# Kernel optimization log

Measured on AMD Instinct MI355X. Metric: run time of the kernel, lower is better.

## Reference

```python
import jax, jax.numpy as jnp
import numpy as np

N_NODES = 100_000
N_FACES = 200_000
IN_CH = 128
OUT_CH = 29  # MLP out = OUT_CH + 3


def setup_inputs() -> dict:
    key = jax.random.key(0)
    k_pos, k_faces, k_ff, k_w1, k_w2 = jax.random.split(key, 5)
    pos = jax.random.normal(k_pos, (N_NODES, 3), dtype=jnp.float32)
    faces = jax.random.randint(k_faces, (N_FACES, 3), 0, N_NODES, dtype=jnp.int32)
    face_features = jax.random.normal(k_ff, (N_FACES, IN_CH), dtype=jnp.float32)
    d_in = IN_CH + 6
    W1 = jax.random.normal(k_w1, (d_in, IN_CH), dtype=jnp.float32) / np.sqrt(d_in)
    b1 = jnp.zeros((IN_CH,), dtype=jnp.float32)
    W2 = jax.random.normal(k_w2, (IN_CH, OUT_CH + 3), dtype=jnp.float32) / np.sqrt(IN_CH)
    b2 = jnp.zeros((OUT_CH + 3,), dtype=jnp.float32)
    return {"pos": pos, "face_features": face_features, "W1": W1, "b1": b1,
            "W2": W2, "b2": b2, "faces": faces}


def reference(pos, face_features, W1, b1, W2, b2, faces):
    def mlp(x):
        return jax.nn.relu(x @ W1 + b1) @ W2 + b2

    p0 = pos[faces[:, 0]]  # [F,3]
    p1 = pos[faces[:, 1]]
    p2 = pos[faces[:, 2]]

    g0 = mlp(jnp.concatenate([p1 - p0, p2 - p0, face_features], axis=1))
    g1 = mlp(jnp.concatenate([p2 - p1, p0 - p1, face_features], axis=1))
    g2 = mlp(jnp.concatenate([p0 - p2, p1 - p2, face_features], axis=1))

    face_features_out = (g0[:, 3:] + g1[:, 3:] + g2[:, 3:]) / 3.0  # [F,OUT_CH]

    # scatter_mean of per-corner deltas onto nodes; torch cat order matches
    # faces.T.flatten() = [faces[:,0], faces[:,1], faces[:,2]]
    vals = jnp.concatenate([g0[:, :3], g1[:, :3], g2[:, :3]], axis=0)  # [3F,3]
    idx = jnp.concatenate([faces[:, 0], faces[:, 1], faces[:, 2]], axis=0)  # [3F]
    sums = jax.ops.segment_sum(vals, idx, num_segments=N_NODES)
    counts = jax.ops.segment_sum(jnp.ones((vals.shape[0],), vals.dtype), idx,
                                 num_segments=N_NODES)
    delta_pos = sums / jnp.clip(counts, 1.0)[:, None]  # [N,3]

    new_pos = pos + delta_pos
    return (delta_pos, new_pos, face_features_out)
```

## Files before the change

### kernel.cpp

```cpp
#include <hip/hip_runtime.h>
#include <hip/hip_bf16.h>

#define N_NODES 100000
#define N_FACES 200000
#define FM 32
#define ROWS 96
#define NTILES (N_FACES / FM)
#define GRID 512
#define FS 136
#define ES 40
#define HS 136
#define W1K 160
#define W2K 128

typedef __attribute__((ext_vector_type(8))) short s8v;
typedef __attribute__((ext_vector_type(4))) short s4v;
typedef __attribute__((ext_vector_type(4))) float f4v;

static __device__ __forceinline__ short f2bf(float x) {
  __hip_bfloat16 h = __float2bfloat16(x);
  short s;
  __builtin_memcpy(&s, &h, 2);
  return s;
}

__global__ __launch_bounds__(256) void prep_kernel(
    const float* __restrict__ W1, const float* __restrict__ W2,
    short* __restrict__ w1t, short* __restrict__ w2t)
{
  int t = blockIdx.x * 256 + threadIdx.x;
  if (t < 128 * W1K) {
    int n = t / W1K, k = t % W1K;
    float v = 0.f;
    if (k < 128) v = W1[(k + 6) * 128 + n];
    else if (k < 134) v = W1[(k - 128) * 128 + n];
    w1t[t] = f2bf(v);
  }
  if (t < 32 * W2K) {
    int o = t / W2K, k = t % W2K;
    w2t[t] = f2bf(W2[k * 32 + o]);
  }
}

__global__ __launch_bounds__(512, 4) void face_kernel(
    const float* __restrict__ pos, const float* __restrict__ ffeat,
    const float* __restrict__ b1, const float* __restrict__ b2,
    const int* __restrict__ faces,
    const short* __restrict__ w1t_g, const short* __restrict__ w2t_g,
    float* __restrict__ out_ff, float* __restrict__ sums, int* __restrict__ cnt)
{
  __shared__ short xff[2][FM * FS];
  __shared__ short xe[2][ROWS * ES];
  __shared__ short hbuf[ROWS * HS];
  __shared__ int   nidb[2][ROWS];
  __shared__ float gsumb[FM * 30];

  const int t = threadIdx.x;
  const int lane = t & 63;
  const int wv = t >> 6;
  const int l15 = lane & 15;
  const int lq = lane >> 4;
  const int kq = lq * 8;
  const int nsel = wv & 1;

  s8v bw1[5], bw2[4];
#pragma unroll
  for (int kc = 0; kc < 5; ++kc)
    bw1[kc] = *(const s8v*)(w1t_g + (wv * 16 + l15) * W1K + kc * 32 + kq);
#pragma unroll
  for (int kk = 0; kk < 4; ++kk)
    bw2[kk] = *(const s8v*)(w2t_g + (nsel * 16 + l15) * W2K + kk * 32 + kq);
  const float b1j = b1[wv * 16 + l15];
  const float b2o = b2[nsel * 16 + l15];

  if (t < 2 * ROWS) {
    int b = t / ROWS, row = t - b * ROWS;
    s8v z = (s8v){0, 0, 0, 0, 0, 0, 0, 0};
    *(unsigned*)&xe[b][row * ES + 6] = 0u;
    *(s8v*)&xe[b][row * ES + 8] = z;
    *(s8v*)&xe[b][row * ES + 16] = z;
    *(s8v*)&xe[b][row * ES + 24] = z;
    *(s8v*)&xe[b][row * ES + 32] = z;
  }

  {
    int fb = blockIdx.x * FM;
    const float* fp = ffeat + ((size_t)(fb + (t >> 4)) << 7) + ((t & 15) << 3);
    f4v v0 = *(const f4v*)fp, v1 = *(const f4v*)(fp + 4);
    s8v s;
    s[0] = f2bf(v0.x); s[1] = f2bf(v0.y); s[2] = f2bf(v0.z); s[3] = f2bf(v0.w);
    s[4] = f2bf(v1.x); s[5] = f2bf(v1.y); s[6] = f2bf(v1.z); s[7] = f2bf(v1.w);
    *(s8v*)&xff[0][(t >> 4) * FS + ((t & 15) << 3)] = s;
    int rt = t - 384;
    if ((unsigned)rt < 96u) {
      int face = fb + (rt & 31), v = rt >> 5;
      int i0 = faces[face * 3 + 0], i1 = faces[face * 3 + 1], i2 = faces[face * 3 + 2];
      int ia = (v == 0) ? i0 : ((v == 1) ? i1 : i2);
      int ib = (v == 0) ? i1 : ((v == 1) ? i2 : i0);
      int ic = (v == 0) ? i2 : ((v == 1) ? i0 : i1);
      float ax = pos[ia * 3], ay = pos[ia * 3 + 1], az = pos[ia * 3 + 2];
      float bx = pos[ib * 3], by = pos[ib * 3 + 1], bz = pos[ib * 3 + 2];
      float cx = pos[ic * 3], cy = pos[ic * 3 + 1], cz = pos[ic * 3 + 2];
      s4v e;
      e[0] = f2bf(bx - ax); e[1] = f2bf(by - ay); e[2] = f2bf(bz - az); e[3] = f2bf(cx - ax);
      *(s4v*)&xe[0][rt * ES] = e;
      unsigned p2 = (unsigned)(unsigned short)f2bf(cy - ay) |
                    ((unsigned)(unsigned short)f2bf(cz - az) << 16);
      *(unsigned*)&xe[0][rt * ES + 4] = p2;
      nidb[0][rt] = ia;
    }
  }
  __syncthreads();

  int iter = 0;
  for (int tile = blockIdx.x; tile < NTILES; tile += GRID, ++iter) {
    const int cur = iter & 1, nxt = cur ^ 1;
    const int fb_c = tile * FM;
    const int tile_n = tile + GRID;
    const bool hn = tile_n < NTILES;
    const int fb_n = tile_n * FM;
    const int rt = t - 384;

    f4v nv0, nv1;
    int ni0 = 0, ni1 = 0, ni2 = 0;
    if (hn) {
      const float* fp = ffeat + ((size_t)(fb_n + (t >> 4)) << 7) + ((t & 15) << 3);
      nv0 = *(const f4v*)fp;
      nv1 = *(const f4v*)(fp + 4);
      if ((unsigned)rt < 96u) {
        int face = fb_n + (rt & 31);
        ni0 = faces[face * 3 + 0]; ni1 = faces[face * 3 + 1]; ni2 = faces[face * 3 + 2];
      }
    }

    f4v acc1[6];
#pragma unroll
    for (int m = 0; m < 6; ++m) acc1[m] = (f4v){0.f, 0.f, 0.f, 0.f};
    const short* xf = &xff[cur][0];
    const short* xeb = &xe[cur][0];
#pragma unroll
    for (int kc = 0; kc < 4; ++kc) {
      s8v a0 = *(const s8v*)&xf[l15 * FS + kc * 32 + kq];
      s8v a1 = *(const s8v*)&xf[(16 + l15) * FS + kc * 32 + kq];
      acc1[0] = __builtin_amdgcn_mfma_f32_16x16x32_bf16(a0, bw1[kc], acc1[0], 0, 0, 0);
      acc1[1] = __builtin_amdgcn_mfma_f32_16x16x32_bf16(a1, bw1[kc], acc1[1], 0, 0, 0);
      acc1[2] = __builtin_amdgcn_mfma_f32_16x16x32_bf16(a0, bw1[kc], acc1[2], 0, 0, 0);
      acc1[3] = __builtin_amdgcn_mfma_f32_16x16x32_bf16(a1, bw1[kc], acc1[3], 0, 0, 0);
      acc1[4] = __builtin_amdgcn_mfma_f32_16x16x32_bf16(a0, bw1[kc], acc1[4], 0, 0, 0);
      acc1[5] = __builtin_amdgcn_mfma_f32_16x16x32_bf16(a1, bw1[kc], acc1[5], 0, 0, 0);
    }
#pragma unroll
    for (int m = 0; m < 6; ++m) {
      s8v a = *(const s8v*)&xeb[(m * 16 + l15) * ES + kq];
      acc1[m] = __builtin_amdgcn_mfma_f32_16x16x32_bf16(a, bw1[4], acc1[m], 0, 0, 0);
    }

    __syncthreads();

    {
      int j = wv * 16 + l15;
#pragma unroll
      for (int m = 0; m < 6; ++m)
#pragma unroll
        for (int r = 0; r < 4; ++r)
          hbuf[(m * 16 + lq * 4 + r) * HS + j] = f2bf(fmaxf(acc1[m][r] + b1j, 0.f));
    }
    for (int e = t; e < FM * 30; e += 512) gsumb[e] = 0.f;

    float pax = 0, pay = 0, paz = 0, pbx = 0, pby = 0, pbz = 0, pcx = 0, pcy = 0, pcz = 0;
    int ia_s = 0, ib_s = 0, ic_s = 0;
    if (hn) {
      s8v s;
      s[0] = f2bf(nv0.x); s[1] = f2bf(nv0.y); s[2] = f2bf(nv0.z); s[3] = f2bf(nv0.w);
      s[4] = f2bf(nv1.x); s[5] = f2bf(nv1.y); s[6] = f2bf(nv1.z); s[7] = f2bf(nv1.w);
      *(s8v*)&xff[nxt][(t >> 4) * FS + ((t & 15) << 3)] = s;
      if ((unsigned)rt < 96u) {
        int v = rt >> 5;
        ia_s = (v == 0) ? ni0 : ((v == 1) ? ni1 : ni2);
        ib_s = (v == 0) ? ni1 : ((v == 1) ? ni2 : ni0);
        ic_s = (v == 0) ? ni2 : ((v == 1) ? ni0 : ni1);
        pax = pos[ia_s * 3]; pay = pos[ia_s * 3 + 1]; paz = pos[ia_s * 3 + 2];
        pbx = pos[ib_s * 3]; pby = pos[ib_s * 3 + 1]; pbz = pos[ib_s * 3 + 2];
        pcx = pos[ic_s * 3]; pcy = pos[ic_s * 3 + 1]; pcz = pos[ic_s * 3 + 2];
      }
    }
    __syncthreads();

#pragma unroll
    for (int p = 0; p < 2; ++p) {
      if (p == 0 || wv < 4) {
        int m = (wv >> 1) + p * 4;
        f4v c2 = (f4v){0.f, 0.f, 0.f, 0.f};
#pragma unroll
        for (int kk = 0; kk < 4; ++kk) {
          s8v a = *(const s8v*)&hbuf[(m * 16 + l15) * HS + kk * 32 + kq];
          c2 = __builtin_amdgcn_mfma_f32_16x16x32_bf16(a, bw2[kk], c2, 0, 0, 0);
        }
        int o = nsel * 16 + l15;
#pragma unroll
        for (int r = 0; r < 4; ++r) {
          int row = m * 16 + lq * 4 + r;
          float g = c2[r] + b2o;
          if (o < 3) {
            int node = nidb[cur][row];
            atomicAdd(&sums[node * 3 + o], g);
            if (o == 0) atomicAdd(&cnt[node], 1);
          } else {
            atomicAdd(&gsumb[(row & 31) * 30 + (o - 3)], g);
          }
        }
      }
    }

    if (hn && (unsigned)rt < 96u) {
      s4v e;
      e[0] = f2bf(pbx - pax); e[1] = f2bf(pby - pay);
      e[2] = f2bf(pbz - paz); e[3] = f2bf(pcx - pax);
      *(s4v*)&xe[nxt][rt * ES] = e;
      unsigned p2 = (unsigned)(unsigned short)f2bf(pcy - pay) |
                    ((unsigned)(unsigned short)f2bf(pcz - paz) << 16);
      *(unsigned*)&xe[nxt][rt * ES + 4] = p2;
      nidb[nxt][rt] = ia_s;
    }
    __syncthreads();

    for (int e = t; e < FM * 29; e += 512) {
      int floc = e / 29, c = e - floc * 29;
      out_ff[((size_t)(fb_c + floc)) * 29 + c] = gsumb[floc * 30 + c] * (1.0f / 3.0f);
    }
  }
}

__global__ __launch_bounds__(256) void node_kernel(
    const float* __restrict__ pos, const float* __restrict__ sums,
    const int* __restrict__ cnt, float* __restrict__ out)
{
  int n = blockIdx.x * 256 + threadIdx.x;
  if (n >= N_NODES) return;
  float c = fmaxf((float)cnt[n], 1.0f);
#pragma unroll
  for (int o = 0; o < 3; ++o) {
    float d = sums[n * 3 + o] / c;
    out[n * 3 + o] = d;
    out[3 * N_NODES + n * 3 + o] = pos[n * 3 + o] + d;
  }
}

extern "C" void kernel_launch(void* const* d_in, const int* in_sizes, int n_in,
                              void* d_out, int out_size, void* d_ws, size_t ws_size,
                              hipStream_t stream) {
  const float* pos   = (const float*)d_in[0];
  const float* ffeat = (const float*)d_in[1];
  const float* W1    = (const float*)d_in[2];
  const float* b1    = (const float*)d_in[3];
  const float* W2    = (const float*)d_in[4];
  const float* b2    = (const float*)d_in[5];
  const int*   faces = (const int*)d_in[6];
  float* out = (float*)d_out;

  float* sums = (float*)d_ws;
  int*   cnt  = (int*)(sums + 3 * N_NODES);
  short* w1t  = (short*)(cnt + N_NODES);
  short* w2t  = w1t + 128 * W1K;

  hipMemsetAsync(d_ws, 0, (size_t)(3 * N_NODES + N_NODES) * 4, stream);
  prep_kernel<<<80, 256, 0, stream>>>(W1, W2, w1t, w2t);
  face_kernel<<<GRID, 512, 0, stream>>>(pos, ffeat, b1, b2, faces, w1t, w2t,
                                        out + 6 * N_NODES, sums, cnt);
  node_kernel<<<(N_NODES + 255) / 256, 256, 0, stream>>>(pos, sums, cnt, out);
}
```

Before: 264.1 us.

## Single-buffer face tiles, coalesce vertex gathers, defer global atomics, raise occupancy

Removes the double-buffered xff/xe/nid shared arrays to cut LDS use, so occupancy rises to 6 blocks per CU and the grid to 768. Face indices are loaded coalesced one per corner (prefetched two tiles ahead), with only one pos gather per thread instead of nine, and edge vectors are built from a shared vertex table. Global scatter atomics move after the final barrier so they overlap with the out_ff store. This adds pipeline depth and register state, and may change the latency-hiding balance.

```diff
diff --git a/kernel.cpp b/kernel.cpp
--- a/kernel.cpp
+++ b/kernel.cpp
@@ -6,7 +6,7 @@
 #define FM 32
 #define ROWS 96
 #define NTILES (N_FACES / FM)
-#define GRID 512
+#define GRID 768
 #define FS 136
 #define ES 40
 #define HS 136
@@ -22,6 +22,9 @@
   short s;
   __builtin_memcpy(&s, &h, 2);
   return s;
+}
+static __device__ __forceinline__ unsigned us(short x) {
+  return (unsigned)(unsigned short)x;
 }
 
 __global__ __launch_bounds__(256) void prep_kernel(
@@ -42,17 +45,18 @@
   }
 }
 
-__global__ __launch_bounds__(512, 4) void face_kernel(
+__global__ __launch_bounds__(512, 6) void face_kernel(
     const float* __restrict__ pos, const float* __restrict__ ffeat,
     const float* __restrict__ b1, const float* __restrict__ b2,
     const int* __restrict__ faces,
     const short* __restrict__ w1t_g, const short* __restrict__ w2t_g,
     float* __restrict__ out_ff, float* __restrict__ sums, int* __restrict__ cnt)
 {
-  __shared__ short xff[2][FM * FS];
-  __shared__ short xe[2][ROWS * ES];
+  __shared__ short xff[FM * FS];
+  __shared__ short xe[ROWS * ES];
   __shared__ short hbuf[ROWS * HS];
-  __shared__ int   nidb[2][ROWS];
+  __shared__ int   fidx[2][ROWS];
+  __shared__ float pvtx[ROWS * 4];
   __shared__ float gsumb[FM * 30];
 
   const int t = threadIdx.x;
@@ -62,6 +66,8 @@
   const int lq = lane >> 4;
   const int kq = lq * 8;
   const int nsel = wv & 1;
+  const int rt = t - 384;
+  const bool rt96 = ((unsigned)rt < 96u);
 
   s8v bw1[5], bw2[4];
 #pragma unroll
@@ -73,16 +79,16 @@
   const float b1j = b1[wv * 16 + l15];
   const float b2o = b2[nsel * 16 + l15];
 
-  if (t < 2 * ROWS) {
-    int b = t / ROWS, row = t - b * ROWS;
+  if (t < ROWS) {
     s8v z = (s8v){0, 0, 0, 0, 0, 0, 0, 0};
-    *(unsigned*)&xe[b][row * ES + 6] = 0u;
-    *(s8v*)&xe[b][row * ES + 8] = z;
-    *(s8v*)&xe[b][row * ES + 16] = z;
-    *(s8v*)&xe[b][row * ES + 24] = z;
-    *(s8v*)&xe[b][row * ES + 32] = z;
-  }
-
+    *(unsigned*)&xe[t * ES + 6] = 0u;
+    *(s8v*)&xe[t * ES + 8] = z;
+    *(s8v*)&xe[t * ES + 16] = z;
+    *(s8v*)&xe[t * ES + 24] = z;
+    *(s8v*)&xe[t * ES + 32] = z;
+  }
+
+  int fvn = 0;
   {
     int fb = blockIdx.x * FM;
     const float* fp = ffeat + ((size_t)(fb + (t >> 4)) << 7) + ((t & 15) << 3);
@@ -90,25 +96,30 @@
     s8v s;
     s[0] = f2bf(v0.x); s[1] = f2bf(v0.y); s[2] = f2bf(v0.z); s[3] = f2bf(v0.w);
     s[4] = f2bf(v1.x); s[5] = f2bf(v1.y); s[6] = f2bf(v1.z); s[7] = f2bf(v1.w);
-    *(s8v*)&xff[0][(t >> 4) * FS + ((t & 15) << 3)] = s;
-    int rt = t - 384;
-    if ((unsigned)rt < 96u) {
-      int face = fb + (rt & 31), v = rt >> 5;
-      int i0 = faces[face * 3 + 0], i1 = faces[face * 3 + 1], i2 = faces[face * 3 + 2];
-      int ia = (v == 0) ? i0 : ((v == 1) ? i1 : i2);
-      int ib = (v == 0) ? i1 : ((v == 1) ? i2 : i0);
-      int ic = (v == 0) ? i2 : ((v == 1) ? i0 : i1);
-      float ax = pos[ia * 3], ay = pos[ia * 3 + 1], az = pos[ia * 3 + 2];
-      float bx = pos[ib * 3], by = pos[ib * 3 + 1], bz = pos[ib * 3 + 2];
-      float cx = pos[ic * 3], cy = pos[ic * 3 + 1], cz = pos[ic * 3 + 2];
-      s4v e;
-      e[0] = f2bf(bx - ax); e[1] = f2bf(by - ay); e[2] = f2bf(bz - az); e[3] = f2bf(cx - ax);
-      *(s4v*)&xe[0][rt * ES] = e;
-      unsigned p2 = (unsigned)(unsigned short)f2bf(cy - ay) |
-                    ((unsigned)(unsigned short)f2bf(cz - az) << 16);
-      *(unsigned*)&xe[0][rt * ES + 4] = p2;
-      nidb[0][rt] = ia;
-    }
+    *(s8v*)&xff[(t >> 4) * FS + ((t & 15) << 3)] = s;
+    if (rt96) {
+      int id = faces[fb * 3 + rt];
+      fidx[0][rt] = id;
+      pvtx[rt * 4 + 0] = pos[id * 3 + 0];
+      pvtx[rt * 4 + 1] = pos[id * 3 + 1];
+      pvtx[rt * 4 + 2] = pos[id * 3 + 2];
+      if (blockIdx.x + GRID < NTILES)
+        fvn = faces[(fb + GRID * FM) * 3 + rt];
+    }
+  }
+  __syncthreads();
+  if (rt96) {
+    int floc = rt / 3, v = rt - floc * 3;
+    int rb = floc * 3 + (v == 2 ? 0 : v + 1);
+    int rc = floc * 3 + (v == 0 ? 2 : v - 1);
+    float ax = pvtx[rt * 4], ay = pvtx[rt * 4 + 1], az = pvtx[rt * 4 + 2];
+    float bx = pvtx[rb * 4], by = pvtx[rb * 4 + 1], bz = pvtx[rb * 4 + 2];
+    float cx = pvtx[rc * 4], cy = pvtx[rc * 4 + 1], cz = pvtx[rc * 4 + 2];
+    int r_ = v * 32 + floc;
+    s4v e;
+    e[0] = f2bf(bx - ax); e[1] = f2bf(by - ay); e[2] = f2bf(bz - az); e[3] = f2bf(cx - ax);
+    *(s4v*)&xe[r_ * ES] = e;
+    *(unsigned*)&xe[r_ * ES + 4] = us(f2bf(cy - ay)) | (us(f2bf(cz - az)) << 16);
   }
   __syncthreads();
 
@@ -118,30 +129,28 @@
     const int fb_c = tile * FM;
     const int tile_n = tile + GRID;
     const bool hn = tile_n < NTILES;
-    const int fb_n = tile_n * FM;
-    const int rt = t - 384;
+    const bool hn2 = tile_n + GRID < NTILES;
 
     f4v nv0, nv1;
-    int ni0 = 0, ni1 = 0, ni2 = 0;
+    float npx = 0.f, npy = 0.f, npz = 0.f;
+    int fvn2 = 0;
     if (hn) {
-      const float* fp = ffeat + ((size_t)(fb_n + (t >> 4)) << 7) + ((t & 15) << 3);
+      const float* fp = ffeat + ((size_t)(tile_n * FM + (t >> 4)) << 7) + ((t & 15) << 3);
       nv0 = *(const f4v*)fp;
       nv1 = *(const f4v*)(fp + 4);
-      if ((unsigned)rt < 96u) {
-        int face = fb_n + (rt & 31);
-        ni0 = faces[face * 3 + 0]; ni1 = faces[face * 3 + 1]; ni2 = faces[face * 3 + 2];
-      }
-    }
+      if (rt96) {
+        npx = pos[fvn * 3 + 0]; npy = pos[fvn * 3 + 1]; npz = pos[fvn * 3 + 2];
+      }
+    }
+    if (hn2 && rt96) fvn2 = faces[(tile_n + GRID) * FM * 3 + rt];
 
     f4v acc1[6];
 #pragma unroll
     for (int m = 0; m < 6; ++m) acc1[m] = (f4v){0.f, 0.f, 0.f, 0.f};
-    const short* xf = &xff[cur][0];
-    const short* xeb = &xe[cur][0];
 #pragma unroll
     for (int kc = 0; kc < 4; ++kc) {
-      s8v a0 = *(const s8v*)&xf[l15 * FS + kc * 32 + kq];
-      s8v a1 = *(const s8v*)&xf[(16 + l15) * FS + kc * 32 + kq];
+      s8v a0 = *(const s8v*)&xff[l15 * FS + kc * 32 + kq];
+      s8v a1 = *(const s8v*)&xff[(16 + l15) * FS + kc * 32 + kq];
       acc1[0] = __builtin_amdgcn_mfma_f32_16x16x32_bf16(a0, bw1[kc], acc1[0], 0, 0, 0);
       acc1[1] = __builtin_amdgcn_mfma_f32_16x16x32_bf16(a1, bw1[kc], acc1[1], 0, 0, 0);
       acc1[2] = __builtin_amdgcn_mfma_f32_16x16x32_bf16(a0, bw1[kc], acc1[2], 0, 0, 0);
@@ -151,7 +160,7 @@
     }
 #pragma unroll
     for (int m = 0; m < 6; ++m) {
-      s8v a = *(const s8v*)&xeb[(m * 16 + l15) * ES + kq];
+      s8v a = *(const s8v*)&xe[(m * 16 + l15) * ES + kq];
       acc1[m] = __builtin_amdgcn_mfma_f32_16x16x32_bf16(a, bw1[4], acc1[m], 0, 0, 0);
     }
 
@@ -166,61 +175,55 @@
           hbuf[(m * 16 + lq * 4 + r) * HS + j] = f2bf(fmaxf(acc1[m][r] + b1j, 0.f));
     }
     for (int e = t; e < FM * 30; e += 512) gsumb[e] = 0.f;
-
-    float pax = 0, pay = 0, paz = 0, pbx = 0, pby = 0, pbz = 0, pcx = 0, pcy = 0, pcz = 0;
-    int ia_s = 0, ib_s = 0, ic_s = 0;
     if (hn) {
       s8v s;
       s[0] = f2bf(nv0.x); s[1] = f2bf(nv0.y); s[2] = f2bf(nv0.z); s[3] = f2bf(nv0.w);
       s[4] = f2bf(nv1.x); s[5] = f2bf(nv1.y); s[6] = f2bf(nv1.z); s[7] = f2bf(nv1.w);
-      *(s8v*)&xff[nxt][(t >> 4) * FS + ((t & 15) << 3)] = s;
-      if ((unsigned)rt < 96u) {
-        int v = rt >> 5;
-        ia_s = (v == 0) ? ni0 : ((v == 1) ? ni1 : ni2);
-        ib_s = (v == 0) ? ni1 : ((v == 1) ? ni2 : ni0);
-        ic_s = (v == 0) ? ni2 : ((v == 1) ? ni0 : ni1);
-        pax = pos[ia_s * 3]; pay = pos[ia_s * 3 + 1]; paz = pos[ia_s * 3 + 2];
-        pbx = pos[ib_s * 3]; pby = pos[ib_s * 3 + 1]; pbz = pos[ib_s * 3 + 2];
-        pcx = pos[ic_s * 3]; pcy = pos[ic_s * 3 + 1]; pcz = pos[ic_s * 3 + 2];
+      *(s8v*)&xff[(t >> 4) * FS + ((t & 15) << 3)] = s;
+      if (rt96) {
+        pvtx[rt * 4 + 0] = npx; pvtx[rt * 4 + 1] = npy; pvtx[rt * 4 + 2] = npz;
+        fidx[nxt][rt] = fvn;
       }
     }
     __syncthreads();
 
-#pragma unroll
-    for (int p = 0; p < 2; ++p) {
-      if (p == 0 || wv < 4) {
-        int m = (wv >> 1) + p * 4;
-        f4v c2 = (f4v){0.f, 0.f, 0.f, 0.f};
-#pragma unroll
-        for (int kk = 0; kk < 4; ++kk) {
-          s8v a = *(const s8v*)&hbuf[(m * 16 + l15) * HS + kk * 32 + kq];
-          c2 = __builtin_amdgcn_mfma_f32_16x16x32_bf16(a, bw2[kk], c2, 0, 0, 0);
-        }
-        int o = nsel * 16 + l15;
-#pragma unroll
-        for (int r = 0; r < 4; ++r) {
-          int row = m * 16 + lq * 4 + r;
-          float g = c2[r] + b2o;
-          if (o < 3) {
-            int node = nidb[cur][row];
-            atomicAdd(&sums[node * 3 + o], g);
-            if (o == 0) atomicAdd(&cnt[node], 1);
-          } else {
-            atomicAdd(&gsumb[(row & 31) * 30 + (o - 3)], g);
-          }
-        }
-      }
-    }
-
-    if (hn && (unsigned)rt < 96u) {
+    f4v c2a = (f4v){0.f, 0.f, 0.f, 0.f}, c2b = (f4v){0.f, 0.f, 0.f, 0.f};
+    const int m0 = wv >> 1, m1 = (wv >> 1) + 4;
+#pragma unroll
+    for (int kk = 0; kk < 4; ++kk) {
+      s8v a = *(const s8v*)&hbuf[(m0 * 16 + l15) * HS + kk * 32 + kq];
+      c2a = __builtin_amdgcn_mfma_f32_16x16x32_bf16(a, bw2[kk], c2a, 0, 0, 0);
+    }
+    if (wv < 4) {
+#pragma unroll
+      for (int kk = 0; kk < 4; ++kk) {
+        s8v a = *(const s8v*)&hbuf[(m1 * 16 + l15) * HS + kk * 32 + kq];
+        c2b = __builtin_amdgcn_mfma_f32_16x16x32_bf16(a, bw2[kk], c2b, 0, 0, 0);
+      }
+    }
+    const int o = nsel * 16 + l15;
+    if (o >= 3) {
+#pragma unroll
+      for (int r = 0; r < 4; ++r)
+        atomicAdd(&gsumb[((m0 * 16 + lq * 4 + r) & 31) * 30 + (o - 3)], c2a[r] + b2o);
+      if (wv < 4) {
+#pragma unroll
+        for (int r = 0; r < 4; ++r)
+          atomicAdd(&gsumb[((m1 * 16 + lq * 4 + r) & 31) * 30 + (o - 3)], c2b[r] + b2o);
+      }
+    }
+    if (hn && rt96) {
+      int floc = rt / 3, v = rt - floc * 3;
+      int rb = floc * 3 + (v == 2 ? 0 : v + 1);
+      int rc = floc * 3 + (v == 0 ? 2 : v - 1);
+      float ax = pvtx[rt * 4], ay = pvtx[rt * 4 + 1], az = pvtx[rt * 4 + 2];
+      float bx = pvtx[rb * 4], by = pvtx[rb * 4 + 1], bz = pvtx[rb * 4 + 2];
+      float cx = pvtx[rc * 4], cy = pvtx[rc * 4 + 1], cz = pvtx[rc * 4 + 2];
+      int r_ = v * 32 + floc;
       s4v e;
-      e[0] = f2bf(pbx - pax); e[1] = f2bf(pby - pay);
-      e[2] = f2bf(pbz - paz); e[3] = f2bf(pcx - pax);
-      *(s4v*)&xe[nxt][rt * ES] = e;
-      unsigned p2 = (unsigned)(unsigned short)f2bf(pcy - pay) |
-                    ((unsigned)(unsigned short)f2bf(pcz - paz) << 16);
-      *(unsigned*)&xe[nxt][rt * ES + 4] = p2;
-      nidb[nxt][rt] = ia_s;
+      e[0] = f2bf(bx - ax); e[1] = f2bf(by - ay); e[2] = f2bf(bz - az); e[3] = f2bf(cx - ax);
+      *(s4v*)&xe[r_ * ES] = e;
+      *(unsigned*)&xe[r_ * ES + 4] = us(f2bf(cy - ay)) | (us(f2bf(cz - az)) << 16);
     }
     __syncthreads();
 
@@ -228,6 +231,25 @@
       int floc = e / 29, c = e - floc * 29;
       out_ff[((size_t)(fb_c + floc)) * 29 + c] = gsumb[floc * 30 + c] * (1.0f / 3.0f);
     }
+    if (o < 3) {
+#pragma unroll
+      for (int r = 0; r < 4; ++r) {
+        int row = m0 * 16 + lq * 4 + r;
+        int nid = fidx[cur][(row & 31) * 3 + (row >> 5)];
+        atomicAdd(&sums[nid * 3 + o], c2a[r] + b2o);
+        if (o == 0) atomicAdd(&cnt[nid], 1);
+      }
+      if (wv < 4) {
+#pragma unroll
+        for (int r = 0; r < 4; ++r) {
+          int row = m1 * 16 + lq * 4 + r;
+          int nid = fidx[cur][(row & 31) * 3 + (row >> 5)];
+          atomicAdd(&sums[nid * 3 + o], c2b[r] + b2o);
+          if (o == 0) atomicAdd(&cnt[nid], 1);
+        }
+      }
+    }
+    fvn = fvn2;
   }
 }
 
```

Result: slower. 313.0 us (+18.5%).
